# Performance work log

Measured on AMD Instinct MI355X. Metric: run time of the kernel, lower is better.

## Reference

```python
import jax, jax.numpy as jnp
import numpy as np
import math

PHI_INV = 2.0 / (1.0 + math.sqrt(5.0))
BATCH, IN_DIM, OUT_DIM = 2048, 512, 128
N_OSC, N_LAYERS, DT, STEPS = 256, 4, 0.1, 10
MU_GATE_FACTOR = 0.5  # module state z=0.5 lies in [MU_1, MU_P) -> gate * 0.5; z < MU_S so no liminal feedback


def setup_inputs() -> dict:
    key = jax.random.key(0)
    ks = jax.random.split(key, 6)
    x = jax.random.normal(ks[0], (BATCH, IN_DIM), jnp.float32)
    W_enc = jax.random.normal(ks[1], (N_OSC, IN_DIM), jnp.float32) / np.sqrt(IN_DIM).astype(np.float32)
    b_enc = jnp.zeros((N_OSC,), jnp.float32)
    K0 = jax.random.normal(ks[2], (N_LAYERS, N_OSC, N_OSC), jnp.float32) * 0.1
    Ks = (K0 + jnp.swapaxes(K0, -1, -2)) / 2  # symmetric init, as in torch
    omegas = jax.random.normal(ks[3], (N_LAYERS, N_OSC), jnp.float32) * 0.1
    K_globals = jnp.full((N_LAYERS,), 0.5, jnp.float32)
    mu_gates = jnp.ones((N_LAYERS,), jnp.float32)
    W_dec = jax.random.normal(ks[4], (OUT_DIM, N_OSC), jnp.float32) / np.sqrt(N_OSC).astype(np.float32)
    b_dec = jnp.zeros((OUT_DIM,), jnp.float32)
    return dict(x=x, W_enc=W_enc, b_enc=b_enc, Ks=Ks, omegas=omegas,
                K_globals=K_globals, mu_gates=mu_gates, W_dec=W_dec, b_dec=b_dec)


def _wrap(t):
    # torch.atan2(sin, cos) phase wrap to (-pi, pi]
    return jnp.arctan2(jnp.sin(t), jnp.cos(t))


def _kuramoto_layer(theta, K, omega, K_global, mu_gate):
    # theta: [B, n]; K: [n, n]
    K_eff = K * (mu_gate * MU_GATE_FACTOR)
    KT = K_eff.T  # so (s @ KT)[b, i] = sum_j K_eff[i, j] * s[b, j]

    def step(th, _):
        s, c = jnp.sin(th), jnp.cos(th)
        # sum_j K[i,j] * sin(th_j - th_i) = cos_i * (K sin)_i - sin_i * (K cos)_i
        coupling_sum = c * (s @ KT) - s * (c @ KT)
        dtheta = omega + (K_global / N_OSC) * coupling_sum
        return _wrap(th + DT * dtheta), None

    theta, _ = jax.lax.scan(step, theta, None, length=STEPS)
    return theta


def reference(x, W_enc, b_enc, Ks, omegas, K_globals, mu_gates, W_dec, b_dec):
    theta = _wrap(x @ W_enc.T + b_enc)  # [B, n]

    def layer(th, params):
        K, om, kg, mg = params
        return _kuramoto_layer(th, K, om, kg, mg), None

    theta, _ = jax.lax.scan(layer, theta, (Ks, omegas, K_globals, mu_gates))
    coherence = jnp.sqrt(jnp.cos(theta).mean(-1) ** 2 + jnp.sin(theta).mean(-1) ** 2)  # [B]
    output = theta @ W_dec.T + b_dec  # [B, out_dim]
    return output, theta, coherence
```

## Files before the change

kernel.cpp:

```cpp
#include <hip/hip_runtime.h>


#define NB 2048
#define NIN 512
#define NOUT 128
#define NOSC 256
#define DTT 0.1f

#define WS_WENC (512*1024)
#define WS_WD   (1024*1024)

typedef _Float16 f16;
typedef _Float16 f16x4 __attribute__((ext_vector_type(4)));
typedef _Float16 f16x8 __attribute__((ext_vector_type(8)));
typedef float f32x4 __attribute__((ext_vector_type(4)));

__device__ __forceinline__ float wrapf(float t) {
    return t - 6.28318530717958648f * rintf(t * 0.159154943091895336f);
}

__global__ __launch_bounds__(256) void helix_prep(
    const float* __restrict__ Ks, const float* __restrict__ Wenc,
    const float* __restrict__ Wdec, char* __restrict__ ws)
{
    const int g = blockIdx.x * 256 + threadIdx.x;
    if (g < 32768) {
        const int ln = g & 63, lg = ln >> 4, lr = ln & 15;
        const int kf = (g >> 6) & 7, nt = (g >> 9) & 15, l = (g >> 13) & 3;
        const float* s = Ks + (((size_t)l * NOSC + nt * 16 + lr) * NOSC + kf * 32 + lg * 8);
        f16x8 o;
        #pragma unroll
        for (int e = 0; e < 8; ++e) o[e] = (f16)s[e];
        *(f16x8*)(ws + (size_t)g * 16) = o;
    } else if (g < 65536) {
        const int q = g - 32768;
        const int ln = q & 63, lg = ln >> 4, lr = ln & 15;
        const int h = (q >> 6) & 1, kf = (q >> 7) & 15, nt = (q >> 11) & 15;
        const float* s = Wenc + ((size_t)(nt * 16 + lr) * NIN + kf * 32 + lg * 8);
        f16x8 o;
        #pragma unroll
        for (int e = 0; e < 8; ++e) {
            float v = s[e];
            f16 hi = (f16)v;
            o[e] = h ? (f16)(v - (float)hi) : hi;
        }
        *(f16x8*)(ws + WS_WENC + (size_t)q * 16) = o;
    } else if (g < 69632) {
        const int q = g - 65536;
        const int ln = q & 63, lg = ln >> 4, lr = ln & 15;
        const int kf = (q >> 6) & 7, nt = (q >> 9) & 7;
        const float* s = Wdec + ((size_t)(nt * 16 + lr) * NOSC + kf * 32 + lg * 8);
        f16x8 o;
        #pragma unroll
        for (int e = 0; e < 8; ++e) o[e] = (f16)s[e];
        *(f16x8*)(ws + WS_WD + (size_t)q * 16) = o;
    }
}

__global__ __launch_bounds__(1024, 4) void helix12(
    const float* __restrict__ x,
    const float* __restrict__ b_enc,
    const float* __restrict__ omegas,
    const float* __restrict__ Kgl,
    const float* __restrict__ mgl,
    const float* __restrict__ b_dec,
    const char* __restrict__ ws,
    float* __restrict__ out)
{
    __shared__ __align__(16) char smem[25600];
    float* th_lds = (float*)(smem + 16384);
    float* cohPS  = (float*)(smem + 24576);
    float* cohPC  = (float*)(smem + 25088);

    const int tid = threadIdx.x;
    const int wv = tid >> 6, ln = tid & 63, lg = ln >> 4, lr = ln & 15;
    const int d  = lr >> 3;
    const int row0 = blockIdx.x * 8;
    const int jb  = 16 * wv + lr;

    float* out_y   = out;
    float* out_th  = out + (size_t)NB * NOUT;
    float* out_coh = out + (size_t)NB * (NOUT + NOSC);

    const int4 zz = make_int4(0, 0, 0, 0);

    float dtccA[4], omL[4];
    #pragma unroll
    for (int l = 0; l < 4; ++l) {
        dtccA[l] = DTT * Kgl[l] * (1.0f / (float)NOSC) * (mgl[l] * 0.5f);
        omL[l]   = DTT * omegas[l * NOSC + jb];
    }

    {
        const int r  = tid >> 7;
        const int j0 = (tid & 127) << 2;
        float4 v = *(const float4*)(x + (size_t)(row0 + r) * NIN + j0);
        float vv[4] = {v.x, v.y, v.z, v.w};
        f16x4 hi, lo;
        #pragma unroll
        for (int e = 0; e < 4; ++e) {
            hi[e] = (f16)vv[e];
            lo[e] = (f16)(vv[e] - (float)hi[e]);
        }
        char* base = smem + (j0 >> 5) * 1024 + ((j0 >> 3) & 3) * 256 + (j0 & 7) * 2;
        *(f16x4*)(base + (2 * r) * 16)     = hi;
        *(f16x4*)(base + (2 * r + 1) * 16) = lo;
    }
    __syncthreads();

    f16x8 BfA[8], BfB[8];
    auto loadK = [&](const int l, f16x8 (&B)[8]) {
        const char* kb = ws + (size_t)l * 131072 + (size_t)wv * 8192 + ln * 16;
        #pragma unroll
        for (int kf = 0; kf < 8; ++kf)
            B[kf] = *(const f16x8*)(kb + kf * 1024);
    };

    float th[2], sv[2], cv[2];
    {
        f32x4 accH = {0,0,0,0}, accL = {0,0,0,0};
        const char* aBase = smem + lg * 256 + lr * 16;
        const char* wE = ws + WS_WENC + (size_t)wv * 32768 + ln * 16;
        #pragma unroll 4
        for (int kf = 0; kf < 16; ++kf) {
            f16x8 a  = *(const f16x8*)(aBase + kf * 1024);
            f16x8 bh = *(const f16x8*)(wE + kf * 2048);
            f16x8 bl = *(const f16x8*)(wE + kf * 2048 + 1024);
            accH = __builtin_amdgcn_mfma_f32_16x16x32_f16(a, bh, accH, 0, 0, 0);
            accL = __builtin_amdgcn_mfma_f32_16x16x32_f16(a, bl, accL, 0, 0, 0);
        }
        loadK(0, BfA);
        const float be = b_enc[jb];
        #pragma unroll
        for (int p = 0; p < 2; ++p) {
            float tval = accH[2*p] + accH[2*p+1] + accL[2*p] + accL[2*p+1] + be;
            th[p] = wrapf(tval);
            __sincosf(th[p], &sv[p], &cv[p]);
        }
    }
    __syncthreads();

    const int rb = lg * 256 + (lr ^ ((lg & 1) << 1)) * 16;
    const int wbase = (jb >> 5) * 1024 + ((jb >> 3) & 3) * 256 + (lr & 7) * 2;
    const int wz0 = wbase + (((4 * lg + 0) ^ (d << 1)) << 4);
    const int wz1 = wbase + (((4 * lg + 1) ^ (d << 1)) << 4);
    const int wz2 = wbase + (((4 * lg + 2) ^ (d << 1)) << 4);
    const int wz3 = wbase + (((4 * lg + 3) ^ (d << 1)) << 4);

    *(f16*)(smem + wz0) = (f16)sv[0];
    *(f16*)(smem + wz1) = (f16)cv[0];
    *(f16*)(smem + wz2) = (f16)sv[1];
    *(f16*)(smem + wz3) = (f16)cv[1];
    __syncthreads();

    auto STEP = [&](const char* Sb, char* Wb, const f16x8 (&Bc)[8],
                    const float om, const float cc) {
        f32x4 accE = {0.f,0.f,0.f,0.f}, accO = {0.f,0.f,0.f,0.f};
        __builtin_amdgcn_s_setprio(1);
        #pragma unroll
        for (int kf = 0; kf < 8; kf += 2) {
            f16x8 a0 = *(const f16x8*)(Sb + kf * 1024 + rb);
            f16x8 a1 = *(const f16x8*)(Sb + (kf + 1) * 1024 + rb);
            accE = __builtin_amdgcn_mfma_f32_16x16x32_f16(a0, Bc[kf],     accE, 0, 0, 0);
            accO = __builtin_amdgcn_mfma_f32_16x16x32_f16(a1, Bc[kf + 1], accO, 0, 0, 0);
        }
        f32x4 acc = accE + accO;
        #pragma unroll
        for (int p = 0; p < 2; ++p) {
            float diff = fmaf(cv[p], acc[2*p], -(sv[p] * acc[2*p+1]));
            th[p] += fmaf(diff, cc, om);
            __sincosf(th[p], &sv[p], &cv[p]);
        }
        *(f16*)(Wb + wz0) = (f16)sv[0];
        *(f16*)(Wb + wz1) = (f16)cv[0];
        *(f16*)(Wb + wz2) = (f16)sv[1];
        *(f16*)(Wb + wz3) = (f16)cv[1];
        __builtin_amdgcn_s_setprio(0);
        asm volatile("s_waitcnt lgkmcnt(0)" ::: "memory");
        __builtin_amdgcn_s_barrier();
    };

    auto runLayer = [&](const f16x8 (&Bc)[8], f16x8 (&Bn)[8], const int lNext,
                        const float om, const float cc) {
        #pragma unroll 1
        for (int p5 = 0; p5 < 5; ++p5) {
            if (p5 == 0 && lNext >= 0) loadK(lNext, Bn);
            STEP(smem,        smem + 8192, Bc, om, cc);
            STEP(smem + 8192, smem,        Bc, om, cc);
        }
    };

    runLayer(BfA, BfB, 1,  omL[0], dtccA[0]);
    runLayer(BfB, BfA, 2,  omL[1], dtccA[1]);
    runLayer(BfA, BfB, 3,  omL[2], dtccA[2]);
    runLayer(BfB, BfA, -1, omL[3], dtccA[3]);

    {
        const int dbase = (jb >> 5) * 1024 + ((jb >> 3) & 3) * 256 + (lr & 7) * 2;
        #pragma unroll
        for (int p = 0; p < 2; ++p) {
            const float wt = wrapf(th[p]);
            th_lds[(2 * lg + p) * NOSC + jb] = wt;
            *(f16*)(smem + dbase + (2 * lg + p) * 16) = (f16)wt;
        }
    }
    #pragma unroll
    for (int p = 0; p < 2; ++p) {
        float pS = sv[p], pC = cv[p];
        pS += __shfl_xor(pS, 1); pC += __shfl_xor(pC, 1);
        pS += __shfl_xor(pS, 2); pC += __shfl_xor(pC, 2);
        pS += __shfl_xor(pS, 4); pC += __shfl_xor(pC, 4);
        pS += __shfl_xor(pS, 8); pC += __shfl_xor(pC, 8);
        if (lr == 0) {
            cohPS[wv * 8 + 2 * lg + p] = pS;
            cohPC[wv * 8 + 2 * lg + p] = pC;
        }
    }
    __syncthreads();

    if (tid < 8)
        *(int4*)(smem + tid * 1024 + 128) = zz;
    if (tid < 512) {
        float4 v = ((const float4*)th_lds)[tid];
        *(float4*)(out_th + (size_t)row0 * NOSC + tid * 4) = v;
    }
    if (tid < 8) {
        float S = 0.f, C = 0.f;
        #pragma unroll
        for (int w2 = 0; w2 < 16; ++w2) {
            S += cohPS[w2 * 8 + tid];
            C += cohPC[w2 * 8 + tid];
        }
        S *= (1.0f / (float)NOSC);
        C *= (1.0f / (float)NOSC);
        out_coh[row0 + tid] = sqrtf(S * S + C * C);
    }
    __syncthreads();

    if (wv < 8) {
        const int rbD = (lr < 8) ? (lg * 256 + lr * 16) : 128;
        f32x4 aD = {0.f, 0.f, 0.f, 0.f};
        #pragma unroll
        for (int kf = 0; kf < 8; ++kf) {
            f16x8 a  = *(const f16x8*)(smem + kf * 1024 + rbD);
            f16x8 bw = *(const f16x8*)(ws + WS_WD + (size_t)wv * 8192 + kf * 1024 + ln * 16);
            aD = __builtin_amdgcn_mfma_f32_16x16x32_f16(a, bw, aD, 0, 0, 0);
        }
        if (lg < 2) {
            const int col = 16 * wv + lr;
            const float bd = b_dec[col];
            #pragma unroll
            for (int e = 0; e < 4; ++e)
                out_y[(size_t)(row0 + 4 * lg + e) * NOUT + col] = aD[e] + bd;
        }
    }
}

extern "C" void kernel_launch(void* const* d_in, const int* in_sizes, int n_in,
                              void* d_out, int out_size, void* d_ws, size_t ws_size,
                              hipStream_t stream) {
    const float* x     = (const float*)d_in[0];
    const float* W_enc = (const float*)d_in[1];
    const float* b_enc = (const float*)d_in[2];
    const float* Ks    = (const float*)d_in[3];
    const float* omg   = (const float*)d_in[4];
    const float* Kgl   = (const float*)d_in[5];
    const float* mgl   = (const float*)d_in[6];
    const float* W_dec = (const float*)d_in[7];
    const float* b_dec = (const float*)d_in[8];
    char* ws = (char*)d_ws;

    helix_prep<<<272, 256, 0, stream>>>(Ks, W_enc, W_dec, ws);
    helix12<<<NB / 8, 1024, 0, stream>>>(x, b_enc, omg, Kgl, mgl, b_dec, ws, (float*)d_out);
}
```

Baseline: 42.83 us.

## Halve block to 512 threads with two oscillator column tiles per wave

Each wave now handles two 16-column oscillator tiles instead of one, so blocks shrink from 16 to 8 waves. Each A fragment read from LDS now feeds two MFMAs, and fewer waves meet at each of the 40 per-step barriers. In exchange each wave holds twice the K fragments in registers (double-buffered across layers), which raises register pressure, and occupancy changes with the new launch bounds.

Measured after the change: 45.71 us. +6.7%, slower.

```diff
diff --git a/kernel.cpp b/kernel.cpp
--- a/kernel.cpp
+++ b/kernel.cpp
@@ -11,7 +11,6 @@
 #define WS_WD   (1024*1024)
 
 typedef _Float16 f16;
-typedef _Float16 f16x4 __attribute__((ext_vector_type(4)));
 typedef _Float16 f16x8 __attribute__((ext_vector_type(8)));
 typedef float f32x4 __attribute__((ext_vector_type(4)));
 
@@ -57,7 +56,7 @@
     }
 }
 
-__global__ __launch_bounds__(1024, 4) void helix12(
+__global__ __launch_bounds__(512, 2) void helix13(
     const float* __restrict__ x,
     const float* __restrict__ b_enc,
     const float* __restrict__ omegas,
@@ -70,13 +69,14 @@
     __shared__ __align__(16) char smem[25600];
     float* th_lds = (float*)(smem + 16384);
     float* cohPS  = (float*)(smem + 24576);
-    float* cohPC  = (float*)(smem + 25088);
+    float* cohPC  = (float*)(smem + 24576 + 256);
 
     const int tid = threadIdx.x;
     const int wv = tid >> 6, ln = tid & 63, lg = ln >> 4, lr = ln & 15;
     const int d  = lr >> 3;
     const int row0 = blockIdx.x * 8;
-    const int jb  = 16 * wv + lr;
+    const int jb0 = 32 * wv + lr;
+    const int jb1 = jb0 + 16;
 
     float* out_y   = out;
     float* out_th  = out + (size_t)NB * NOUT;
@@ -84,104 +84,138 @@
 
     const int4 zz = make_int4(0, 0, 0, 0);
 
-    float dtccA[4], omL[4];
+    float dtccA[4];
+    float2 omL[4];
     #pragma unroll
     for (int l = 0; l < 4; ++l) {
         dtccA[l] = DTT * Kgl[l] * (1.0f / (float)NOSC) * (mgl[l] * 0.5f);
-        omL[l]   = DTT * omegas[l * NOSC + jb];
+        omL[l] = make_float2(DTT * omegas[l * NOSC + jb0],
+                             DTT * omegas[l * NOSC + jb1]);
     }
 
     {
-        const int r  = tid >> 7;
-        const int j0 = (tid & 127) << 2;
-        float4 v = *(const float4*)(x + (size_t)(row0 + r) * NIN + j0);
-        float vv[4] = {v.x, v.y, v.z, v.w};
-        f16x4 hi, lo;
-        #pragma unroll
-        for (int e = 0; e < 4; ++e) {
+        const int r  = wv;
+        const int j0 = ln * 8;
+        const float* xp = x + (size_t)(row0 + r) * NIN + j0;
+        float4 v0 = *(const float4*)xp;
+        float4 v1 = *(const float4*)(xp + 4);
+        float vv[8] = {v0.x, v0.y, v0.z, v0.w, v1.x, v1.y, v1.z, v1.w};
+        f16x8 hi, lo;
+        #pragma unroll
+        for (int e = 0; e < 8; ++e) {
             hi[e] = (f16)vv[e];
             lo[e] = (f16)(vv[e] - (float)hi[e]);
         }
-        char* base = smem + (j0 >> 5) * 1024 + ((j0 >> 3) & 3) * 256 + (j0 & 7) * 2;
-        *(f16x4*)(base + (2 * r) * 16)     = hi;
-        *(f16x4*)(base + (2 * r + 1) * 16) = lo;
-    }
-    __syncthreads();
-
-    f16x8 BfA[8], BfB[8];
-    auto loadK = [&](const int l, f16x8 (&B)[8]) {
-        const char* kb = ws + (size_t)l * 131072 + (size_t)wv * 8192 + ln * 16;
-        #pragma unroll
-        for (int kf = 0; kf < 8; ++kf)
-            B[kf] = *(const f16x8*)(kb + kf * 1024);
+        char* base = smem + (j0 >> 5) * 1024 + ((j0 >> 3) & 3) * 256;
+        *(f16x8*)(base + (2 * r) * 16)     = hi;
+        *(f16x8*)(base + (2 * r + 1) * 16) = lo;
+    }
+    __syncthreads();
+
+    f16x8 BfA[2][8], BfB[2][8];
+    auto loadK = [&](const int l, f16x8 (&B)[2][8]) {
+        #pragma unroll
+        for (int u = 0; u < 2; ++u) {
+            const char* kb = ws + (size_t)l * 131072 + (size_t)(2 * wv + u) * 8192 + ln * 16;
+            #pragma unroll
+            for (int kf = 0; kf < 8; ++kf)
+                B[u][kf] = *(const f16x8*)(kb + kf * 1024);
+        }
     };
 
-    float th[2], sv[2], cv[2];
+    float th[2][2], sv[2][2], cv[2][2];
     {
-        f32x4 accH = {0,0,0,0}, accL = {0,0,0,0};
+        f32x4 accH[2] = {{0,0,0,0},{0,0,0,0}};
+        f32x4 accL[2] = {{0,0,0,0},{0,0,0,0}};
         const char* aBase = smem + lg * 256 + lr * 16;
-        const char* wE = ws + WS_WENC + (size_t)wv * 32768 + ln * 16;
+        const char* wE0 = ws + WS_WENC + (size_t)(2 * wv) * 32768 + ln * 16;
+        const char* wE1 = wE0 + 32768;
         #pragma unroll 4
         for (int kf = 0; kf < 16; ++kf) {
-            f16x8 a  = *(const f16x8*)(aBase + kf * 1024);
-            f16x8 bh = *(const f16x8*)(wE + kf * 2048);
-            f16x8 bl = *(const f16x8*)(wE + kf * 2048 + 1024);
-            accH = __builtin_amdgcn_mfma_f32_16x16x32_f16(a, bh, accH, 0, 0, 0);
-            accL = __builtin_amdgcn_mfma_f32_16x16x32_f16(a, bl, accL, 0, 0, 0);
+            f16x8 a   = *(const f16x8*)(aBase + kf * 1024);
+            f16x8 bh0 = *(const f16x8*)(wE0 + kf * 2048);
+            f16x8 bl0 = *(const f16x8*)(wE0 + kf * 2048 + 1024);
+            accH[0] = __builtin_amdgcn_mfma_f32_16x16x32_f16(a, bh0, accH[0], 0, 0, 0);
+            accL[0] = __builtin_amdgcn_mfma_f32_16x16x32_f16(a, bl0, accL[0], 0, 0, 0);
+            f16x8 bh1 = *(const f16x8*)(wE1 + kf * 2048);
+            f16x8 bl1 = *(const f16x8*)(wE1 + kf * 2048 + 1024);
+            accH[1] = __builtin_amdgcn_mfma_f32_16x16x32_f16(a, bh1, accH[1], 0, 0, 0);
+            accL[1] = __builtin_amdgcn_mfma_f32_16x16x32_f16(a, bl1, accL[1], 0, 0, 0);
         }
         loadK(0, BfA);
-        const float be = b_enc[jb];
-        #pragma unroll
-        for (int p = 0; p < 2; ++p) {
-            float tval = accH[2*p] + accH[2*p+1] + accL[2*p] + accL[2*p+1] + be;
-            th[p] = wrapf(tval);
-            __sincosf(th[p], &sv[p], &cv[p]);
+        #pragma unroll
+        for (int u = 0; u < 2; ++u) {
+            const float be = b_enc[u ? jb1 : jb0];
+            #pragma unroll
+            for (int p = 0; p < 2; ++p) {
+                float tval = accH[u][2*p] + accH[u][2*p+1]
+                           + accL[u][2*p] + accL[u][2*p+1] + be;
+                th[u][p] = wrapf(tval);
+                __sincosf(th[u][p], &sv[u][p], &cv[u][p]);
+            }
         }
     }
     __syncthreads();
 
     const int rb = lg * 256 + (lr ^ ((lg & 1) << 1)) * 16;
-    const int wbase = (jb >> 5) * 1024 + ((jb >> 3) & 3) * 256 + (lr & 7) * 2;
-    const int wz0 = wbase + (((4 * lg + 0) ^ (d << 1)) << 4);
-    const int wz1 = wbase + (((4 * lg + 1) ^ (d << 1)) << 4);
-    const int wz2 = wbase + (((4 * lg + 2) ^ (d << 1)) << 4);
-    const int wz3 = wbase + (((4 * lg + 3) ^ (d << 1)) << 4);
-
-    *(f16*)(smem + wz0) = (f16)sv[0];
-    *(f16*)(smem + wz1) = (f16)cv[0];
-    *(f16*)(smem + wz2) = (f16)sv[1];
-    *(f16*)(smem + wz3) = (f16)cv[1];
-    __syncthreads();
-
-    auto STEP = [&](const char* Sb, char* Wb, const f16x8 (&Bc)[8],
-                    const float om, const float cc) {
-        f32x4 accE = {0.f,0.f,0.f,0.f}, accO = {0.f,0.f,0.f,0.f};
+    int wz[2][4];
+    #pragma unroll
+    for (int u = 0; u < 2; ++u) {
+        const int jbu = u ? jb1 : jb0;
+        const int wbase = (jbu >> 5) * 1024 + ((jbu >> 3) & 3) * 256 + (lr & 7) * 2;
+        #pragma unroll
+        for (int q = 0; q < 4; ++q)
+            wz[u][q] = wbase + (((4 * lg + q) ^ (d << 1)) << 4);
+    }
+
+    #pragma unroll
+    for (int u = 0; u < 2; ++u) {
+        *(f16*)(smem + wz[u][0]) = (f16)sv[u][0];
+        *(f16*)(smem + wz[u][1]) = (f16)cv[u][0];
+        *(f16*)(smem + wz[u][2]) = (f16)sv[u][1];
+        *(f16*)(smem + wz[u][3]) = (f16)cv[u][1];
+    }
+    __syncthreads();
+
+    auto STEP = [&](const char* Sb, char* Wb, const f16x8 (&Bc)[2][8],
+                    const float2 om, const float cc) {
+        f32x4 aE0 = {0.f,0.f,0.f,0.f}, aO0 = {0.f,0.f,0.f,0.f};
+        f32x4 aE1 = {0.f,0.f,0.f,0.f}, aO1 = {0.f,0.f,0.f,0.f};
         __builtin_amdgcn_s_setprio(1);
         #pragma unroll
         for (int kf = 0; kf < 8; kf += 2) {
             f16x8 a0 = *(const f16x8*)(Sb + kf * 1024 + rb);
             f16x8 a1 = *(const f16x8*)(Sb + (kf + 1) * 1024 + rb);
-            accE = __builtin_amdgcn_mfma_f32_16x16x32_f16(a0, Bc[kf],     accE, 0, 0, 0);
-            accO = __builtin_amdgcn_mfma_f32_16x16x32_f16(a1, Bc[kf + 1], accO, 0, 0, 0);
-        }
-        f32x4 acc = accE + accO;
+            aE0 = __builtin_amdgcn_mfma_f32_16x16x32_f16(a0, Bc[0][kf],     aE0, 0, 0, 0);
+            aE1 = __builtin_amdgcn_mfma_f32_16x16x32_f16(a0, Bc[1][kf],     aE1, 0, 0, 0);
+            aO0 = __builtin_amdgcn_mfma_f32_16x16x32_f16(a1, Bc[0][kf + 1], aO0, 0, 0, 0);
+            aO1 = __builtin_amdgcn_mfma_f32_16x16x32_f16(a1, Bc[1][kf + 1], aO1, 0, 0, 0);
+        }
+        f32x4 acc0 = aE0 + aO0;
+        f32x4 acc1 = aE1 + aO1;
         #pragma unroll
         for (int p = 0; p < 2; ++p) {
-            float diff = fmaf(cv[p], acc[2*p], -(sv[p] * acc[2*p+1]));
-            th[p] += fmaf(diff, cc, om);
-            __sincosf(th[p], &sv[p], &cv[p]);
-        }
-        *(f16*)(Wb + wz0) = (f16)sv[0];
-        *(f16*)(Wb + wz1) = (f16)cv[0];
-        *(f16*)(Wb + wz2) = (f16)sv[1];
-        *(f16*)(Wb + wz3) = (f16)cv[1];
+            float diff0 = fmaf(cv[0][p], acc0[2*p], -(sv[0][p] * acc0[2*p+1]));
+            th[0][p] += fmaf(diff0, cc, om.x);
+            __sincosf(th[0][p], &sv[0][p], &cv[0][p]);
+            float diff1 = fmaf(cv[1][p], acc1[2*p], -(sv[1][p] * acc1[2*p+1]));
+            th[1][p] += fmaf(diff1, cc, om.y);
+            __sincosf(th[1][p], &sv[1][p], &cv[1][p]);
+        }
+        #pragma unroll
+        for (int u = 0; u < 2; ++u) {
+            *(f16*)(Wb + wz[u][0]) = (f16)sv[u][0];
+            *(f16*)(Wb + wz[u][1]) = (f16)cv[u][0];
+            *(f16*)(Wb + wz[u][2]) = (f16)sv[u][1];
+            *(f16*)(Wb + wz[u][3]) = (f16)cv[u][1];
+        }
         __builtin_amdgcn_s_setprio(0);
         asm volatile("s_waitcnt lgkmcnt(0)" ::: "memory");
         __builtin_amdgcn_s_barrier();
     };
 
-    auto runLayer = [&](const f16x8 (&Bc)[8], f16x8 (&Bn)[8], const int lNext,
-                        const float om, const float cc) {
+    auto runLayer = [&](const f16x8 (&Bc)[2][8], f16x8 (&Bn)[2][8], const int lNext,
+                        const float2 om, const float cc) {
         #pragma unroll 1
         for (int p5 = 0; p5 < 5; ++p5) {
             if (p5 == 0 && lNext >= 0) loadK(lNext, Bn);
@@ -195,18 +229,21 @@
     runLayer(BfA, BfB, 3,  omL[2], dtccA[2]);
     runLayer(BfB, BfA, -1, omL[3], dtccA[3]);
 
-    {
-        const int dbase = (jb >> 5) * 1024 + ((jb >> 3) & 3) * 256 + (lr & 7) * 2;
+    #pragma unroll
+    for (int u = 0; u < 2; ++u) {
+        const int jbu = u ? jb1 : jb0;
+        const int dbase = (jbu >> 5) * 1024 + ((jbu >> 3) & 3) * 256 + (lr & 7) * 2;
         #pragma unroll
         for (int p = 0; p < 2; ++p) {
-            const float wt = wrapf(th[p]);
-            th_lds[(2 * lg + p) * NOSC + jb] = wt;
+            const float wt = wrapf(th[u][p]);
+            th_lds[(2 * lg + p) * NOSC + jbu] = wt;
             *(f16*)(smem + dbase + (2 * lg + p) * 16) = (f16)wt;
         }
     }
     #pragma unroll
     for (int p = 0; p < 2; ++p) {
-        float pS = sv[p], pC = cv[p];
+        float pS = sv[0][p] + sv[1][p];
+        float pC = cv[0][p] + cv[1][p];
         pS += __shfl_xor(pS, 1); pC += __shfl_xor(pC, 1);
         pS += __shfl_xor(pS, 2); pC += __shfl_xor(pC, 2);
         pS += __shfl_xor(pS, 4); pC += __shfl_xor(pC, 4);
@@ -220,14 +257,14 @@
 
     if (tid < 8)
         *(int4*)(smem + tid * 1024 + 128) = zz;
-    if (tid < 512) {
+    {
         float4 v = ((const float4*)th_lds)[tid];
         *(float4*)(out_th + (size_t)row0 * NOSC + tid * 4) = v;
     }
     if (tid < 8) {
         float S = 0.f, C = 0.f;
         #pragma unroll
-        for (int w2 = 0; w2 < 16; ++w2) {
+        for (int w2 = 0; w2 < 8; ++w2) {
             S += cohPS[w2 * 8 + tid];
             C += cohPC[w2 * 8 + tid];
         }
@@ -237,7 +274,7 @@
     }
     __syncthreads();
 
-    if (wv < 8) {
+    {
         const int rbD = (lr < 8) ? (lg * 256 + lr * 16) : 128;
         f32x4 aD = {0.f, 0.f, 0.f, 0.f};
         #pragma unroll
@@ -271,5 +308,5 @@
     char* ws = (char*)d_ws;
 
     helix_prep<<<272, 256, 0, stream>>>(Ks, W_enc, W_dec, ws);
-    helix12<<<NB / 8, 1024, 0, stream>>>(x, b_enc, omg, Kgl, mgl, b_dec, ws, (float*)d_out);
+    helix13<<<NB / 8, 512, 0, stream>>>(x, b_enc, omg, Kgl, mgl, b_dec, ws, (float*)d_out);
 }
```
